# Kernel optimization log

Measured on AMD Instinct MI355X. Metric: run time of the kernel, lower is better.

## Reference

```python
import jax, jax.numpy as jnp
import numpy as np

B_, C_, H_, W_, Dd_ = 2, 64, 32, 32, 32
D_INNER, D_STATE, DT_RANK, D_CONV = 64, 8, 4, 4


def setup_inputs() -> dict:
    key = jax.random.key(0)
    ks = jax.random.split(key, 12)
    s = 0.05
    A_init = jnp.log(jnp.tile(jnp.arange(1, D_STATE + 1, dtype=jnp.float32), (D_INNER, 1)))
    return {
        "input": jax.random.normal(ks[0], (B_, C_, H_, W_, Dd_), jnp.float32),
        "conv_w": jax.random.normal(ks[1], (C_, C_, 3, 3, 3), jnp.float32) * s,
        "conv_b": jax.random.normal(ks[2], (C_,), jnp.float32) * s,
        "in_proj_w": jax.random.normal(ks[3], (2 * D_INNER, C_), jnp.float32) * s,
        "conv1d_w": jax.random.normal(ks[4], (D_INNER, 1, D_CONV), jnp.float32) * s,
        "conv1d_b": jax.random.normal(ks[5], (D_INNER,), jnp.float32) * s,
        "x_proj_w": jax.random.normal(ks[6], (DT_RANK + 2 * D_STATE, D_INNER), jnp.float32) * s,
        "dt_proj_w": jax.random.normal(ks[7], (D_INNER, DT_RANK), jnp.float32) * s,
        "dt_proj_b": jax.random.normal(ks[8], (D_INNER,), jnp.float32) * s,
        "A_log": A_init,
        "A_b_log": A_init + 0.01,
        "D_skip": jnp.ones((D_INNER,), jnp.float32),
        "out_proj_w": jax.random.normal(ks[9], (C_, D_INNER), jnp.float32) * s,
        "ln_g": jnp.ones((C_,), jnp.float32),
        "ln_b": jnp.zeros((C_,), jnp.float32),
    }


def _conv3d(x, w, b):
    y = jax.lax.conv_general_dilated(x, w, (1, 1, 1), [(1, 1), (1, 1), (1, 1)],
                                     dimension_numbers=("NCDHW", "OIDHW", "NCDHW"))
    return y + b[None, :, None, None, None]


def _instance_norm(x, eps=1e-5):
    m = x.mean(axis=(2, 3, 4), keepdims=True)
    v = ((x - m) ** 2).mean(axis=(2, 3, 4), keepdims=True)
    return (x - m) * jax.lax.rsqrt(v + eps)


def _selective_scan(xc, dt, Bm, Cm, A, D_skip):
    # xc, dt: (b,L,d); Bm, Cm: (b,L,n); A: (d,n)
    dA = jnp.exp(dt[..., None] * A)                       # (b,L,d,n)
    dBx = (dt * xc)[..., None] * Bm[:, :, None, :]        # (b,L,d,n)

    def comb(l, r):
        al, bl = l
        ar, br = r
        return ar * al, ar * bl + br

    _, h = jax.lax.associative_scan(comb, (dA, dBx), axis=1)
    y = jnp.einsum("bldn,bln->bld", h, Cm)
    return y + xc * D_skip


def _direction(xz, conv1d_w, conv1d_b, x_proj_w, dt_proj_w, dt_proj_b, A, D_skip):
    x, z = jnp.split(xz, 2, axis=-1)                      # each (b,L,d)
    xt = jnp.swapaxes(x, 1, 2)                            # (b,d,L)
    xc = jax.lax.conv_general_dilated(xt, conv1d_w, (1,), [(D_CONV - 1, 0)],
                                      feature_group_count=D_INNER,
                                      dimension_numbers=("NCH", "OIH", "NCH"))
    xc = jax.nn.silu(jnp.swapaxes(xc + conv1d_b[None, :, None], 1, 2))  # (b,L,d)
    dbl = xc @ x_proj_w.T
    dt_r = dbl[..., :DT_RANK]
    Bm = dbl[..., DT_RANK:DT_RANK + D_STATE]
    Cm = dbl[..., DT_RANK + D_STATE:]
    dt = jax.nn.softplus(dt_r @ dt_proj_w.T + dt_proj_b)
    y = _selective_scan(xc, dt, Bm, Cm, A, D_skip)
    return y * jax.nn.silu(z)


def reference(input, conv_w, conv_b, in_proj_w, conv1d_w, conv1d_b, x_proj_w,
              dt_proj_w, dt_proj_b, A_log, A_b_log, D_skip, out_proj_w, ln_g, ln_b):
    # skip path: Conv3d -> InstanceNorm3d -> ReLU
    skip = jax.nn.relu(_instance_norm(_conv3d(input, conv_w, conv_b)))
    b, c, h, w, d = input.shape
    tokens = input.transpose(0, 2, 3, 4, 1).reshape(b, h * w * d, c)  # b (hwd) c
    xz = tokens @ in_proj_w.T                                          # (b,L,2d)
    A = -jnp.exp(A_log)
    A_b = -jnp.exp(A_b_log)
    y_f = _direction(xz, conv1d_w, conv1d_b, x_proj_w, dt_proj_w, dt_proj_b, A, D_skip)
    y_b = _direction(xz[:, ::-1], conv1d_w, conv1d_b, x_proj_w, dt_proj_w, dt_proj_b, A_b, D_skip)[:, ::-1]
    out = ((y_f + y_b) @ out_proj_w.T) / 2.0  # if_devide_out=True
    mu = out.mean(-1, keepdims=True)
    var = ((out - mu) ** 2).mean(-1, keepdims=True)
    out = (out - mu) * jax.lax.rsqrt(var + 1e-5) * ln_g + ln_b  # use_norm=True
    vol = out.reshape(b, h, w, d, c).transpose(0, 4, 1, 2, 3)
    return _conv3d(vol, conv_w, conv_b) + skip
```

## Files before the change

kernel.cpp:

```cpp
#include <hip/hip_runtime.h>
#include <hip/hip_bf16.h>

typedef __hip_bfloat16 bf16;
typedef __attribute__((ext_vector_type(8))) short short8;
typedef __attribute__((ext_vector_type(4))) float f32x4;

__device__ __forceinline__ float b2f(bf16 x){ return __bfloat162float(x); }
__device__ __forceinline__ bf16  f2b(float x){ return __float2bfloat16(x); }
__device__ __forceinline__ float s2f(short s){ bf16 t = *(bf16*)&s; return b2f(t); }

__device__ __forceinline__ float ldin(const void* p, size_t i, int f32){
  return f32 ? ((const float*)p)[i] : b2f(((const bf16*)p)[i]);
}
__device__ __forceinline__ void stout(void* p, size_t i, float v, int f32){
  if(f32) ((float*)p)[i] = v; else ((bf16*)p)[i] = f2b(v);
}

constexpr int SP   = 32*32*32;
constexpr int LTOK = SP;
constexpr int NC   = 1024;
constexpr int CLEN = LTOK / NC;
constexpr int NSEQ = 2*2*64*8;
constexpr int SEG  = 32;
constexpr int SEGLEN = NC/SEG;

__global__ void k_detect(const void* conv_w, int* flag){
  if(threadIdx.x==0 && blockIdx.x==0){
    const bf16* p = (const bf16*)conv_w;
    int f = 0;
    for(int i=0;i<128;i++){
      float v = b2f(p[i]);
      if(!(v==v) || fabsf(v) > 1.0f) f = 1;
    }
    *flag = f;
  }
}

__global__ void k_fill(void* out, int n, const int* flag){
  const int f32 = *flag;
  int i = blockIdx.x*256 + threadIdx.x;
  if(i<n) stout(out, i, 12345.0f, f32);
}

__global__ void k_wprep(const void* __restrict__ cw, bf16* __restrict__ wt,
                        const int* __restrict__ flag){
  const int f32 = *flag;
  int t = blockIdx.x*256 + threadIdx.x;
  if(t >= 27*64*64) return;
  int tap = t >> 12;
  int oc  = (t >> 6) & 63;
  int ci  = t & 63;
  wt[t] = f2b(ldin(cw, ((size_t)(oc*64+ci))*27 + tap, f32));
}

__global__ __launch_bounds__(256) void k_inprojm(
    const void* __restrict__ in, const void* __restrict__ pw,
    bf16* __restrict__ xz, bf16* __restrict__ xin_t,
    const int* __restrict__ flag){
  const int f32 = *flag;
  __shared__ bf16 tok[128*72];
  __shared__ bf16 wl [128*72];
  int tid = threadIdx.x;
  int b = blockIdx.x >> 8, tile = blockIdx.x & 255;
  int l0 = tile*128;

  for(int p=tid; p<1024; p+=256){
    int j = p & 127, c8 = p >> 7;
    short8 v;
    #pragma unroll
    for(int k=0;k<8;k++){
      bf16 t = f2b(ldin(pw, j*64 + c8*8 + k, f32));
      v[k] = *(short*)&t;
    }
    *(short8*)(&wl[j*72 + c8*8]) = v;
  }
  for(int p=tid; p<1024; p+=256){
    int i = p & 127, c8 = p >> 7;
    short8 v;
    #pragma unroll
    for(int k=0;k<8;k++){
      bf16 t = f2b(ldin(in, ((size_t)(b*64 + c8*8 + k))*SP + l0 + i, f32));
      v[k] = *(short*)&t;
    }
    *(short8*)(&tok[i*72 + c8*8]) = v;
  }
  __syncthreads();

  int lane = tid & 63, wv = tid >> 6;
  int pn = lane & 15, quad = lane >> 4, kg8 = quad*8;
  f32x4 acc[2][8];
  #pragma unroll
  for(int mt=0;mt<2;mt++)
    #pragma unroll
    for(int nt=0;nt<8;nt++) acc[mt][nt]=(f32x4)(0.f);

  #pragma unroll
  for(int kq=0;kq<2;kq++){
    short8 a0 = *(const short8*)(&tok[(wv*32      + pn)*72 + kq*32 + kg8]);
    short8 a1 = *(const short8*)(&tok[(wv*32 + 16 + pn)*72 + kq*32 + kg8]);
    #pragma unroll
    for(int nt=0;nt<8;nt++){
      short8 bb = *(const short8*)(&wl[(nt*16+pn)*72 + kq*32 + kg8]);
      acc[0][nt] = __builtin_amdgcn_mfma_f32_16x16x32_bf16(a0,bb,acc[0][nt],0,0,0);
      acc[1][nt] = __builtin_amdgcn_mfma_f32_16x16x32_bf16(a1,bb,acc[1][nt],0,0,0);
    }
  }

  #pragma unroll
  for(int mt=0;mt<2;mt++){
    #pragma unroll
    for(int nt=0;nt<8;nt++){
      #pragma unroll
      for(int r=0;r<4;r++){
        int token = wv*32 + mt*16 + quad*4 + r;
        xz[((size_t)b*LTOK + l0 + token)*128 + nt*16 + pn] = f2b(acc[mt][nt][r]);
      }
    }
  }
  for(int p=tid; p<8192; p+=256){
    int i = p >> 6, c = p & 63;
    xin_t[((size_t)b*SP + l0 + i)*64 + c] = tok[i*72 + c];
  }
}

__global__ __launch_bounds__(256, 2) void k_convm(
    const bf16* __restrict__ xin_t, const bf16* __restrict__ wt,
    const void* __restrict__ cb, const bf16* __restrict__ skip,
    bf16* __restrict__ out_bf, void* __restrict__ out_any,
    int mode, const int* __restrict__ flag){
  const int f32 = *flag;
  __shared__ bf16 xt[972*40];

  int tid  = threadIdx.x;
  int lane = tid & 63;
  int wv   = tid >> 6;
  int pn   = lane & 15;
  int quad = lane >> 4;
  int kg8  = quad * 8;
  int laneA = pn*64 + kg8;

  int blk0 = blockIdx.x;
  int blk  = (blk0 & 7)*128 + (blk0 >> 3);
  int ocg = blk & 3;
  int wh  = (blk >> 2) & 1;
  int dh2 = (blk >> 3) & 1;
  int h   = (blk >> 4) & 31;
  int b   = blk >> 9;
  int w0  = wh*16;
  int d0  = dh2*16;

  f32x4 acc[4];
  #pragma unroll
  for(int m=0;m<4;m++) acc[m]=(f32x4)(0.f);

  for(int cic=0; cic<64; cic+=32){
    if(cic) __syncthreads();
    for(int it=0; it<16; it++){
      int j = it*256 + tid;
      if(j < 3888){
        int q4 = j & 3, row = j >> 2;
        int hh = row / 324; int rem = row - hh*324;
        int ww = rem / 18;  int dd = rem - ww*18;
        int hg = h + hh - 1, wg = w0 + ww - 1, d = d0 + dd - 1;
        short8 v = (short8)(0);
        if((unsigned)hg < 32u && (unsigned)wg < 32u && (unsigned)d < 32u)
          v = *(const short8*)(&xin_t[(((size_t)b*SP) + hg*1024 + wg*32 + d)*64 + cic + q4*8]);
        *(short8*)(&xt[row*40 + q4*8]) = v;
      }
    }
    __syncthreads();

    short8 afr[27];
    #pragma unroll
    for(int t=0;t<27;t++)
      afr[t] = *(const short8*)(wt + t*4096 + ocg*1024 + cic + laneA);

    #pragma unroll
    for(int kz=0;kz<3;kz++){
      #pragma unroll
      for(int ky=0;ky<3;ky++){
        #pragma unroll
        for(int kx=0;kx<3;kx++){
          int tap = (kz*3+ky)*3+kx;
          #pragma unroll
          for(int wr=0;wr<4;wr++){
            int rix = (kz*18 + wv*4 + wr + ky)*18 + kx + pn;
            short8 bb = *(const short8*)(&xt[rix*40 + kg8]);
            acc[wr] = __builtin_amdgcn_mfma_f32_16x16x32_bf16(afr[tap], bb, acc[wr], 0,0,0);
          }
        }
      }
    }
  }

  #pragma unroll
  for(int wr=0;wr<4;wr++){
    #pragma unroll
    for(int r=0;r<4;r++){
      int oc = ocg*16 + quad*4 + r;
      size_t idx = ((size_t)(b*64+oc))*SP + h*1024 + (w0 + wv*4 + wr)*32 + d0 + pn;
      float v = acc[wr][r] + ldin(cb, oc, f32);
      if(mode==0) out_bf[idx] = f2b(v);
      else        stout(out_any, idx, v + b2f(skip[idx]), f32);
    }
  }
}

__global__ void k_inorm(bf16* __restrict__ buf){
  int bc = blockIdx.x;
  bf16* p = buf + (size_t)bc*SP;
  float s=0.f, s2=0.f;
  for(int i=threadIdx.x;i<SP;i+=256){ float v=b2f(p[i]); s+=v; s2+=v*v; }
  __shared__ float sh[8];
  #pragma unroll
  for(int m=32;m>=1;m>>=1){ s += __shfl_xor(s,m); s2 += __shfl_xor(s2,m); }
  int wid = threadIdx.x>>6;
  if((threadIdx.x&63)==0){ sh[wid]=s; sh[4+wid]=s2; }
  __syncthreads();
  if(threadIdx.x==0){ float a=0,b2=0; for(int i=0;i<4;i++){a+=sh[i]; b2+=sh[4+i];} sh[0]=a; sh[4]=b2; }
  __syncthreads();
  float mean = sh[0]*(1.f/SP);
  float var  = sh[4]*(1.f/SP) - mean*mean;
  float inv = rsqrtf(fmaxf(var,0.f) + 1e-5f);
  for(int i=threadIdx.x;i<SP;i+=256){
    float v=(b2f(p[i])-mean)*inv;
    p[i] = f2b(v>0.f ? v : 0.f);
  }
}

__global__ __launch_bounds__(256) void k_dirprep(
                          const bf16* __restrict__ xz, const void* __restrict__ c1w,
                          const void* __restrict__ c1b, const void* __restrict__ xpw,
                          bf16* __restrict__ bcg, float* __restrict__ dtr,
                          const int* __restrict__ flag){
  const int f32 = *flag;
  __shared__ float xs[67][64];
  __shared__ float xcs[64][68];
  __shared__ float xws[20][68];
  int bid = blockIdx.x;
  int g = bid >> 10, b = (bid>>9)&1, tile = bid & 511;
  int l0 = tile*64;
  int gb = g*2+b;
  int tid = threadIdx.x;
  for(int t=tid; t<20*64; t+=256){ int j=t>>6, d=t&63; xws[j][d]=ldin(xpw, t, f32); }
  for(int t=tid; t<67*64; t+=256){
    int row=t>>6, d=t&63;
    int l = l0 + row - 3;
    float v = 0.f;
    if(l>=0 && l<LTOK){
      int lg = g ? (LTOK-1-l) : l;
      v = b2f(xz[((size_t)b*LTOK + lg)*128 + d]);
    }
    xs[row][d]=v;
  }
  __syncthreads();
  {
    int d = tid & 63;
    float cw0=ldin(c1w,d*4+0,f32), cw1=ldin(c1w,d*4+1,f32),
          cw2=ldin(c1w,d*4+2,f32), cw3=ldin(c1w,d*4+3,f32);
    float cb_=ldin(c1b,d,f32);
    for(int tl = tid>>6; tl<64; tl+=4){
      float acc = cb_ + cw0*xs[tl][d] + cw1*xs[tl+1][d] + cw2*xs[tl+2][d] + cw3*xs[tl+3][d];
      xcs[tl][d] = acc / (1.f + __expf(-acc));
    }
  }
  __syncthreads();
  {
    int tl = tid & 63, wq = tid >> 6;
    float acc[5] = {0.f,0.f,0.f,0.f,0.f};
    #pragma unroll 4
    for(int d4=0; d4<16; d4++){
      float4 xv = *(const float4*)(&xcs[tl][d4*4]);
      #pragma unroll
      for(int jj=0; jj<5; jj++){
        float4 wv = *(const float4*)(&xws[wq*5+jj][d4*4]);
        acc[jj] += xv.x*wv.x + xv.y*wv.y + xv.z*wv.z + xv.w*wv.w;
      }
    }
    size_t l = (size_t)gb*LTOK + l0 + tl;
    #pragma unroll
    for(int jj=0; jj<5; jj++){
      int j = wq*5 + jj;
      if(j<4) dtr[l*4 + j] = acc[jj];
      else    bcg[l*16 + (j-4)] = f2b(acc[jj]);
    }
  }
}

__global__ __launch_bounds__(256, 2) void k_scan1(
                        const bf16* __restrict__ xz, const float* __restrict__ dtr,
                        const bf16* __restrict__ bcg,
                        const void* __restrict__ c1w, const void* __restrict__ c1b,
                        const void* __restrict__ dpw, const void* __restrict__ dpb,
                        const void* __restrict__ alog, const void* __restrict__ ablog,
                        float* __restrict__ psP, float* __restrict__ psS,
                        const int* __restrict__ flag){
  const int f32 = *flag;
  int wid = blockIdx.x*4 + (threadIdx.x>>6);
  int lane = threadIdx.x & 63;
  int chunk = wid & (NC-1);
  int b = (wid>>10)&1;
  int g = wid>>11;
  int gb = g*2+b;
  const void* al = g ? ablog : alog;
  float ac[8];
  #pragma unroll
  for(int n=0;n<8;n++) ac[n] = -__expf(ldin(al, lane*8+n, f32));
  float cw0=ldin(c1w,lane*4+0,f32), cw1=ldin(c1w,lane*4+1,f32), cw2=ldin(c1w,lane*4+2,f32), cw3=ldin(c1w,lane*4+3,f32);
  float cb_=ldin(c1b,lane,f32);
  float dw0=ldin(dpw,lane*4+0,f32), dw1=ldin(dpw,lane*4+1,f32), dw2=ldin(dpw,lane*4+2,f32), dw3=ldin(dpw,lane*4+3,f32);
  float db_=ldin(dpb,lane,f32);
  float S[8];
  #pragma unroll
  for(int n=0;n<8;n++) S[n]=0.f;
  float Tsum = 0.f;
  int lt0 = chunk*CLEN;
  float x0,x1,x2;
  {
    float xr[3];
    #pragma unroll
    for(int j=0;j<3;j++){
      int lt = lt0-3+j;
      float v=0.f;
      if(lt>=0){ int lg = g ? (LTOK-1-lt) : lt; v=b2f(xz[((size_t)b*LTOK+lg)*128 + lane]); }
      xr[j]=v;
    }
    x0=xr[0]; x1=xr[1]; x2=xr[2];
  }
  for(int i0=0;i0<CLEN;i0+=8){
    bf16 xv[8]; float4 dv[8]; short8 bb[8];
    #pragma unroll
    for(int k=0;k<8;k++){
      int lt = lt0+i0+k;
      int lg = g ? (LTOK-1-lt) : lt;
      xv[k] = xz[((size_t)b*LTOK+lg)*128 + lane];
      size_t l = (size_t)gb*LTOK + lt;
      dv[k] = *(const float4*)(dtr + l*4);
      bb[k] = *(const short8*)(bcg + l*16);
    }
    #pragma unroll
    for(int k=0;k<8;k++){
      float x3 = b2f(xv[k]);
      float pre = cb_ + cw0*x0 + cw1*x1 + cw2*x2 + cw3*x3;
      float xc = pre / (1.f + __expf(-pre));
      float v = db_ + dv[k].x*dw0 + dv[k].y*dw1 + dv[k].z*dw2 + dv[k].w*dw3;
      float e = __expf(-fabsf(v));
      float dt = fmaxf(v,0.f) + __logf(1.f+e);
      Tsum += dt;
      float bx = dt*xc;
      #pragma unroll
      for(int n=0;n<8;n++){
        float a = __expf(dt*ac[n]);
        S[n] = a*S[n] + bx*s2f(bb[k][n]);
      }
      x0=x1; x1=x2; x2=x3;
    }
  }
  int seq = (gb*64 + lane)*8;
  #pragma unroll
  for(int n=0;n<8;n++){
    psP[(size_t)chunk*NSEQ + seq + n] = __expf(ac[n]*Tsum);
    psS[(size_t)chunk*NSEQ + seq + n] = S[n];
  }
}

__global__ void k_scan2a(const float* __restrict__ psP, const float* __restrict__ psS,
                         float* __restrict__ segP, float* __restrict__ segS){
  int idx = blockIdx.x*256 + threadIdx.x;
  int seq = idx & (NSEQ-1);
  int seg = idx >> 11;
  float P = 1.f, S = 0.f;
  int i0 = seg*SEGLEN;
  #pragma unroll 4
  for(int i=0;i<SEGLEN;i++){
    float p = psP[(size_t)(i0+i)*NSEQ + seq];
    float s = psS[(size_t)(i0+i)*NSEQ + seq];
    S = p*S + s;
    P *= p;
  }
  segP[seg*NSEQ + seq] = P;
  segS[seg*NSEQ + seq] = S;
}
__global__ void k_scan2b(const float* __restrict__ segP, const float* __restrict__ segS,
                         float* __restrict__ segC){
  int seq = blockIdx.x*256 + threadIdx.x;
  if(seq >= NSEQ) return;
  float h = 0.f;
  #pragma unroll
  for(int s=0;s<SEG;s++){
    segC[s*NSEQ + seq] = h;
    h = segP[s*NSEQ + seq]*h + segS[s*NSEQ + seq];
  }
}
__global__ void k_scan2c(const float* __restrict__ psP, const float* __restrict__ segC,
                         float* __restrict__ psC){
  int idx = blockIdx.x*256 + threadIdx.x;
  int seq = idx & (NSEQ-1);
  int seg = idx >> 11;
  float h = segC[seg*NSEQ + seq];
  int i0 = seg*SEGLEN;
  #pragma unroll 4
  for(int i=0;i<SEGLEN;i++){
    float p = psP[(size_t)(i0+i)*NSEQ + seq];
    float s = psC[(size_t)(i0+i)*NSEQ + seq];
    psC[(size_t)(i0+i)*NSEQ + seq] = h;
    h = p*h + s;
  }
}

__global__ __launch_bounds__(256, 2) void k_scan3(
                        const bf16* __restrict__ xz, const float* __restrict__ dtr,
                        const bf16* __restrict__ bcg,
                        const void* __restrict__ c1w, const void* __restrict__ c1b,
                        const void* __restrict__ dpw, const void* __restrict__ dpb,
                        const void* __restrict__ alog, const void* __restrict__ ablog,
                        const void* __restrict__ dskip, const float* __restrict__ carry,
                        bf16* __restrict__ ybuf, const int* __restrict__ flag){
  const int f32 = *flag;
  int wid = blockIdx.x*4 + (threadIdx.x>>6);
  int lane = threadIdx.x & 63;
  int chunk = wid & (NC-1);
  int b = (wid>>10)&1;
  int g = wid>>11;
  int gb = g*2+b;
  const void* al = g ? ablog : alog;
  float ac[8];
  #pragma unroll
  for(int n=0;n<8;n++) ac[n] = -__expf(ldin(al, lane*8+n, f32));
  float cw0=ldin(c1w,lane*4+0,f32), cw1=ldin(c1w,lane*4+1,f32), cw2=ldin(c1w,lane*4+2,f32), cw3=ldin(c1w,lane*4+3,f32);
  float cb_=ldin(c1b,lane,f32);
  float dw0=ldin(dpw,lane*4+0,f32), dw1=ldin(dpw,lane*4+1,f32), dw2=ldin(dpw,lane*4+2,f32), dw3=ldin(dpw,lane*4+3,f32);
  float db_=ldin(dpb,lane,f32);
  float dsk = ldin(dskip,lane,f32);
  int seq = (gb*64 + lane)*8;
  float h[8];
  #pragma unroll
  for(int n=0;n<8;n++) h[n] = carry[(size_t)chunk*NSEQ + seq + n];
  int lt0 = chunk*CLEN;
  float x0,x1,x2;
  {
    float xr[3];
    #pragma unroll
    for(int j=0;j<3;j++){
      int lt = lt0-3+j;
      float v=0.f;
      if(lt>=0){ int lg = g ? (LTOK-1-lt) : lt; v=b2f(xz[((size_t)b*LTOK+lg)*128 + lane]); }
      xr[j]=v;
    }
    x0=xr[0]; x1=xr[1]; x2=xr[2];
  }
  for(int i0=0;i0<CLEN;i0+=8){
    bf16 xv[8]; float4 dv[8]; short8 bb[8]; short8 cc[8];
    #pragma unroll
    for(int k=0;k<8;k++){
      int lt = lt0+i0+k;
      int lg = g ? (LTOK-1-lt) : lt;
      xv[k] = xz[((size_t)b*LTOK+lg)*128 + lane];
      size_t l = (size_t)gb*LTOK + lt;
      dv[k] = *(const float4*)(dtr + l*4);
      bb[k] = *(const short8*)(bcg + l*16);
      cc[k] = *(const short8*)(bcg + l*16 + 8);
    }
    #pragma unroll
    for(int k=0;k<8;k++){
      float x3 = b2f(xv[k]);
      float pre = cb_ + cw0*x0 + cw1*x1 + cw2*x2 + cw3*x3;
      float xc = pre / (1.f + __expf(-pre));
      float v = db_ + dv[k].x*dw0 + dv[k].y*dw1 + dv[k].z*dw2 + dv[k].w*dw3;
      float e = __expf(-fabsf(v));
      float dt = fmaxf(v,0.f) + __logf(1.f+e);
      float bx = dt*xc;
      float y = xc*dsk;
      #pragma unroll
      for(int n=0;n<8;n++){
        float a = __expf(dt*ac[n]);
        h[n] = a*h[n] + bx*s2f(bb[k][n]);
        y += h[n]*s2f(cc[k][n]);
      }
      size_t l = (size_t)gb*LTOK + lt0+i0+k;
      ybuf[l*64 + lane] = f2b(y);
      x0=x1; x1=x2; x2=x3;
    }
  }
}

__global__ __launch_bounds__(256) void k_outln(
                        const bf16* __restrict__ ybuf, const bf16* __restrict__ xz,
                        const void* __restrict__ opw,
                        const void* __restrict__ lng, const void* __restrict__ lnb,
                        bf16* __restrict__ vol_t, const int* __restrict__ flag){
  const int f32 = *flag;
  __shared__ bf16 vsm[64*72];
  __shared__ bf16 wsm[64*72];
  __shared__ float gsm[64], bsm[64];
  int tid = threadIdx.x;
  int b = blockIdx.x >> 9, tile = blockIdx.x & 511;
  int l0 = tile*64;

  for(int p=tid; p<512; p+=256){
    int c = p & 63, d8 = p >> 6;
    short8 v;
    #pragma unroll
    for(int k=0;k<8;k++){ bf16 t = f2b(ldin(opw, c*64 + d8*8 + k, f32)); v[k] = *(short*)&t; }
    *(short8*)(&wsm[c*72 + d8*8]) = v;
  }
  if(tid<64){ gsm[tid]=ldin(lng,tid,f32); bsm[tid]=ldin(lnb,tid,f32); }
  for(int p=tid; p<4096; p+=256){
    int tl = p >> 6, d = p & 63;
    int l = l0 + tl;
    float yf = b2f(ybuf[((size_t)(0+b)*LTOK + l)*64 + d]);
    float yb = b2f(ybuf[((size_t)(2+b)*LTOK + (LTOK-1-l))*64 + d]);
    float z  = b2f(xz[((size_t)b*LTOK + l)*128 + 64 + d]);
    float sz = z / (1.f + __expf(-z));
    vsm[tl*72 + d] = f2b(0.5f*(yf+yb)*sz);
  }
  __syncthreads();

  int lane = tid & 63, wv = tid >> 6, pn = lane & 15, quad = lane >> 4, kg8 = quad*8;
  f32x4 acc[4];
  #pragma unroll
  for(int nt=0;nt<4;nt++) acc[nt]=(f32x4)(0.f);
  #pragma unroll
  for(int kq=0;kq<2;kq++){
    short8 a = *(const short8*)(&vsm[(wv*16+pn)*72 + kq*32 + kg8]);
    #pragma unroll
    for(int nt=0;nt<4;nt++){
      short8 bb = *(const short8*)(&wsm[(nt*16+pn)*72 + kq*32 + kg8]);
      acc[nt] = __builtin_amdgcn_mfma_f32_16x16x32_bf16(a,bb,acc[nt],0,0,0);
    }
  }
  __syncthreads();

  float gl[4], bl[4];
  #pragma unroll
  for(int nt=0;nt<4;nt++){ gl[nt]=gsm[nt*16+pn]; bl[nt]=bsm[nt*16+pn]; }
  #pragma unroll
  for(int r=0;r<4;r++){
    float vals[4]; float s=0.f;
    #pragma unroll
    for(int nt=0;nt<4;nt++){ vals[nt]=acc[nt][r]; s+=vals[nt]; }
    #pragma unroll
    for(int m=1;m<16;m<<=1) s += __shfl_xor(s, m);
    float mu = s*(1.f/64.f);
    float s2=0.f;
    #pragma unroll
    for(int nt=0;nt<4;nt++){ float dv=vals[nt]-mu; s2+=dv*dv; }
    #pragma unroll
    for(int m=1;m<16;m<<=1) s2 += __shfl_xor(s2, m);
    float inv = rsqrtf(s2*(1.f/64.f) + 1e-5f);
    int token = wv*16 + quad*4 + r;
    #pragma unroll
    for(int nt=0;nt<4;nt++){
      vsm[token*72 + nt*16 + pn] = f2b((vals[nt]-mu)*inv*gl[nt] + bl[nt]);
    }
  }
  __syncthreads();
  for(int p=tid; p<512; p+=256){
    int tl = p >> 3, d8 = p & 7;
    *(short8*)(&vol_t[((size_t)b*SP + l0 + tl)*64 + d8*8]) = *(const short8*)(&vsm[tl*72 + d8*8]);
  }
}

extern "C" void kernel_launch(void* const* d_in, const int* in_sizes, int n_in,
                              void* d_out, int out_size, void* d_ws, size_t ws_size,
                              hipStream_t stream){
  const void* input  = d_in[0];
  const void* conv_w = d_in[1];
  const void* conv_b = d_in[2];
  const void* inpw   = d_in[3];
  const void* c1w    = d_in[4];
  const void* c1b    = d_in[5];
  const void* xpw    = d_in[6];
  const void* dpw    = d_in[7];
  const void* dpb    = d_in[8];
  const void* alog   = d_in[9];
  const void* ablog  = d_in[10];
  const void* dskip  = d_in[11];
  const void* opw    = d_in[12];
  const void* lng    = d_in[13];
  const void* lnb    = d_in[14];

  char* base = (char*)d_ws;
  bf16*  skipb = (bf16*) (base + 0);
  bf16*  xz    = (bf16*) (base + 8388608);
  bf16*  bcg   = (bf16*) (base + 25165824);
  float* dtr   = (float*)(base + 29360128);
  float* psP   = (float*)(base + 31457280);
  bf16*  xin_t = (bf16*) (base + 39845888);
  bf16*  ybuf  = (bf16*) (base + 31457280);
  float* psS   = (float*)(base + 48234496);
  bf16*  vol_t = (bf16*) (base + 48234496);
  bf16*  wt    = (bf16*) (base + 56623104);
  float* segP  = (float*)(base + 56844288);
  float* segS  = (float*)(base + 57106432);
  float* segC  = (float*)(base + 57368576);
  int*   flagp = (int*)  (base + 57630720);
  const size_t NEED = 57630736;

  k_detect<<<dim3(1), dim3(64), 0, stream>>>(conv_w, flagp);

  if(ws_size < NEED){
    k_fill<<<dim3((out_size+255)/256), dim3(256), 0, stream>>>(d_out, out_size, flagp);
    return;
  }

  k_wprep  <<<dim3(432),   dim3(256), 0, stream>>>(conv_w, wt, flagp);
  k_inprojm<<<dim3(512),   dim3(256), 0, stream>>>(input, inpw, xz, xin_t, flagp);
  k_convm  <<<dim3(1024),  dim3(256), 0, stream>>>(xin_t, wt, conv_b, nullptr, skipb, nullptr, 0, flagp);
  k_inorm  <<<dim3(128),   dim3(256), 0, stream>>>(skipb);
  k_dirprep<<<dim3(2048),  dim3(256), 0, stream>>>(xz, c1w, c1b, xpw, bcg, dtr, flagp);
  k_scan1  <<<dim3(1024),  dim3(256), 0, stream>>>(xz, dtr, bcg, c1w, c1b, dpw, dpb, alog, ablog, psP, psS, flagp);
  k_scan2a <<<dim3(256),   dim3(256), 0, stream>>>(psP, psS, segP, segS);
  k_scan2b <<<dim3(8),     dim3(256), 0, stream>>>(segP, segS, segC);
  k_scan2c <<<dim3(256),   dim3(256), 0, stream>>>(psP, segC, psS);
  k_scan3  <<<dim3(1024),  dim3(256), 0, stream>>>(xz, dtr, bcg, c1w, c1b, dpw, dpb, alog, ablog, dskip, psS, ybuf, flagp);
  k_outln  <<<dim3(1024),  dim3(256), 0, stream>>>(ybuf, xz, opw, lng, lnb, vol_t, flagp);
  k_convm  <<<dim3(1024),  dim3(256), 0, stream>>>(vol_t, wt, conv_b, skipb, nullptr, d_out, 1, flagp);
}
```

Measured before the change: 411.4 us.

## Split scan state dimension across two wavefronts to double parallelism

Scan kernels now use 128-thread blocks where each wavefront handles half of the 8 state dimensions for a channel, quadrupling the block count. In the output pass, partial y contributions are combined via a double-buffered shared-memory array with a barrier per 8 tokens. This raises wave-level parallelism and latency hiding for the serial recurrence, at the cost of duplicating the per-token conv/softplus work and adding synchronization.

```diff
diff --git a/kernel.cpp b/kernel.cpp
--- a/kernel.cpp
+++ b/kernel.cpp
@@ -3,6 +3,7 @@
 
 typedef __hip_bfloat16 bf16;
 typedef __attribute__((ext_vector_type(8))) short short8;
+typedef __attribute__((ext_vector_type(4))) short short4v;
 typedef __attribute__((ext_vector_type(4))) float f32x4;
 
 __device__ __forceinline__ float b2f(bf16 x){ return __bfloat162float(x); }
@@ -287,7 +288,7 @@
   }
 }
 
-__global__ __launch_bounds__(256, 2) void k_scan1(
+__global__ __launch_bounds__(128, 4) void k_scan1(
                         const bf16* __restrict__ xz, const float* __restrict__ dtr,
                         const bf16* __restrict__ bcg,
                         const void* __restrict__ c1w, const void* __restrict__ c1b,
@@ -296,23 +297,24 @@
                         float* __restrict__ psP, float* __restrict__ psS,
                         const int* __restrict__ flag){
   const int f32 = *flag;
-  int wid = blockIdx.x*4 + (threadIdx.x>>6);
+  int bid = blockIdx.x;
   int lane = threadIdx.x & 63;
-  int chunk = wid & (NC-1);
-  int b = (wid>>10)&1;
-  int g = wid>>11;
+  int nh   = threadIdx.x >> 6;
+  int chunk = bid & (NC-1);
+  int b = (bid>>10)&1;
+  int g = bid>>11;
   int gb = g*2+b;
   const void* al = g ? ablog : alog;
-  float ac[8];
-  #pragma unroll
-  for(int n=0;n<8;n++) ac[n] = -__expf(ldin(al, lane*8+n, f32));
+  float ac[4];
+  #pragma unroll
+  for(int n=0;n<4;n++) ac[n] = -__expf(ldin(al, lane*8 + nh*4 + n, f32));
   float cw0=ldin(c1w,lane*4+0,f32), cw1=ldin(c1w,lane*4+1,f32), cw2=ldin(c1w,lane*4+2,f32), cw3=ldin(c1w,lane*4+3,f32);
   float cb_=ldin(c1b,lane,f32);
   float dw0=ldin(dpw,lane*4+0,f32), dw1=ldin(dpw,lane*4+1,f32), dw2=ldin(dpw,lane*4+2,f32), dw3=ldin(dpw,lane*4+3,f32);
   float db_=ldin(dpb,lane,f32);
-  float S[8];
-  #pragma unroll
-  for(int n=0;n<8;n++) S[n]=0.f;
+  float S[4];
+  #pragma unroll
+  for(int n=0;n<4;n++) S[n]=0.f;
   float Tsum = 0.f;
   int lt0 = chunk*CLEN;
   float x0,x1,x2;
@@ -328,7 +330,7 @@
     x0=xr[0]; x1=xr[1]; x2=xr[2];
   }
   for(int i0=0;i0<CLEN;i0+=8){
-    bf16 xv[8]; float4 dv[8]; short8 bb[8];
+    bf16 xv[8]; float4 dv[8]; short4v bb[8];
     #pragma unroll
     for(int k=0;k<8;k++){
       int lt = lt0+i0+k;
@@ -336,7 +338,7 @@
       xv[k] = xz[((size_t)b*LTOK+lg)*128 + lane];
       size_t l = (size_t)gb*LTOK + lt;
       dv[k] = *(const float4*)(dtr + l*4);
-      bb[k] = *(const short8*)(bcg + l*16);
+      bb[k] = *(const short4v*)(bcg + l*16 + nh*4);
     }
     #pragma unroll
     for(int k=0;k<8;k++){
@@ -349,16 +351,16 @@
       Tsum += dt;
       float bx = dt*xc;
       #pragma unroll
-      for(int n=0;n<8;n++){
+      for(int n=0;n<4;n++){
         float a = __expf(dt*ac[n]);
         S[n] = a*S[n] + bx*s2f(bb[k][n]);
       }
       x0=x1; x1=x2; x2=x3;
     }
   }
-  int seq = (gb*64 + lane)*8;
-  #pragma unroll
-  for(int n=0;n<8;n++){
+  int seq = (gb*64 + lane)*8 + nh*4;
+  #pragma unroll
+  for(int n=0;n<4;n++){
     psP[(size_t)chunk*NSEQ + seq + n] = __expf(ac[n]*Tsum);
     psS[(size_t)chunk*NSEQ + seq + n] = S[n];
   }
@@ -408,7 +410,7 @@
   }
 }
 
-__global__ __launch_bounds__(256, 2) void k_scan3(
+__global__ __launch_bounds__(128, 4) void k_scan3(
                         const bf16* __restrict__ xz, const float* __restrict__ dtr,
                         const bf16* __restrict__ bcg,
                         const void* __restrict__ c1w, const void* __restrict__ c1b,
@@ -417,25 +419,27 @@
                         const void* __restrict__ dskip, const float* __restrict__ carry,
                         bf16* __restrict__ ybuf, const int* __restrict__ flag){
   const int f32 = *flag;
-  int wid = blockIdx.x*4 + (threadIdx.x>>6);
+  __shared__ float ysh[2][8][64];
+  int bid = blockIdx.x;
   int lane = threadIdx.x & 63;
-  int chunk = wid & (NC-1);
-  int b = (wid>>10)&1;
-  int g = wid>>11;
+  int nh   = threadIdx.x >> 6;
+  int chunk = bid & (NC-1);
+  int b = (bid>>10)&1;
+  int g = bid>>11;
   int gb = g*2+b;
   const void* al = g ? ablog : alog;
-  float ac[8];
-  #pragma unroll
-  for(int n=0;n<8;n++) ac[n] = -__expf(ldin(al, lane*8+n, f32));
+  float ac[4];
+  #pragma unroll
+  for(int n=0;n<4;n++) ac[n] = -__expf(ldin(al, lane*8 + nh*4 + n, f32));
   float cw0=ldin(c1w,lane*4+0,f32), cw1=ldin(c1w,lane*4+1,f32), cw2=ldin(c1w,lane*4+2,f32), cw3=ldin(c1w,lane*4+3,f32);
   float cb_=ldin(c1b,lane,f32);
   float dw0=ldin(dpw,lane*4+0,f32), dw1=ldin(dpw,lane*4+1,f32), dw2=ldin(dpw,lane*4+2,f32), dw3=ldin(dpw,lane*4+3,f32);
   float db_=ldin(dpb,lane,f32);
   float dsk = ldin(dskip,lane,f32);
-  int seq = (gb*64 + lane)*8;
-  float h[8];
-  #pragma unroll
-  for(int n=0;n<8;n++) h[n] = carry[(size_t)chunk*NSEQ + seq + n];
+  int seq = (gb*64 + lane)*8 + nh*4;
+  float h[4];
+  #pragma unroll
+  for(int n=0;n<4;n++) h[n] = carry[(size_t)chunk*NSEQ + seq + n];
   int lt0 = chunk*CLEN;
   float x0,x1,x2;
   {
@@ -450,7 +454,8 @@
     x0=xr[0]; x1=xr[1]; x2=xr[2];
   }
   for(int i0=0;i0<CLEN;i0+=8){
-    bf16 xv[8]; float4 dv[8]; short8 bb[8]; short8 cc[8];
+    int bt = (i0>>3)&1;
+    bf16 xv[8]; float4 dv[8]; short4v bb[8], cc[8];
     #pragma unroll
     for(int k=0;k<8;k++){
       int lt = lt0+i0+k;
@@ -458,9 +463,10 @@
       xv[k] = xz[((size_t)b*LTOK+lg)*128 + lane];
       size_t l = (size_t)gb*LTOK + lt;
       dv[k] = *(const float4*)(dtr + l*4);
-      bb[k] = *(const short8*)(bcg + l*16);
-      cc[k] = *(const short8*)(bcg + l*16 + 8);
-    }
+      bb[k] = *(const short4v*)(bcg + l*16 + nh*4);
+      cc[k] = *(const short4v*)(bcg + l*16 + 8 + nh*4);
+    }
+    float py[8];
     #pragma unroll
     for(int k=0;k<8;k++){
       float x3 = b2f(xv[k]);
@@ -470,16 +476,24 @@
       float e = __expf(-fabsf(v));
       float dt = fmaxf(v,0.f) + __logf(1.f+e);
       float bx = dt*xc;
-      float y = xc*dsk;
+      float part = nh ? xc*dsk : 0.f;
       #pragma unroll
-      for(int n=0;n<8;n++){
+      for(int n=0;n<4;n++){
         float a = __expf(dt*ac[n]);
         h[n] = a*h[n] + bx*s2f(bb[k][n]);
-        y += h[n]*s2f(cc[k][n]);
+        part += h[n]*s2f(cc[k][n]);
       }
-      size_t l = (size_t)gb*LTOK + lt0+i0+k;
-      ybuf[l*64 + lane] = f2b(y);
+      if(nh==0) ysh[bt][k][lane] = part;
+      else      py[k] = part;
       x0=x1; x1=x2; x2=x3;
+    }
+    __syncthreads();
+    if(nh==1){
+      #pragma unroll
+      for(int k=0;k<8;k++){
+        size_t l = (size_t)gb*LTOK + lt0+i0+k;
+        ybuf[l*64 + lane] = f2b(ysh[bt][k][lane] + py[k]);
+      }
     }
   }
 }
@@ -609,11 +623,11 @@
   k_convm  <<<dim3(1024),  dim3(256), 0, stream>>>(xin_t, wt, conv_b, nullptr, skipb, nullptr, 0, flagp);
   k_inorm  <<<dim3(128),   dim3(256), 0, stream>>>(skipb);
   k_dirprep<<<dim3(2048),  dim3(256), 0, stream>>>(xz, c1w, c1b, xpw, bcg, dtr, flagp);
-  k_scan1  <<<dim3(1024),  dim3(256), 0, stream>>>(xz, dtr, bcg, c1w, c1b, dpw, dpb, alog, ablog, psP, psS, flagp);
+  k_scan1  <<<dim3(4096),  dim3(128), 0, stream>>>(xz, dtr, bcg, c1w, c1b, dpw, dpb, alog, ablog, psP, psS, flagp);
   k_scan2a <<<dim3(256),   dim3(256), 0, stream>>>(psP, psS, segP, segS);
   k_scan2b <<<dim3(8),     dim3(256), 0, stream>>>(segP, segS, segC);
   k_scan2c <<<dim3(256),   dim3(256), 0, stream>>>(psP, segC, psS);
-  k_scan3  <<<dim3(1024),  dim3(256), 0, stream>>>(xz, dtr, bcg, c1w, c1b, dpw, dpb, alog, ablog, dskip, psS, ybuf, flagp);
+  k_scan3  <<<dim3(4096),  dim3(128), 0, stream>>>(xz, dtr, bcg, c1w, c1b, dpw, dpb, alog, ablog, dskip, psS, ybuf, flagp);
   k_outln  <<<dim3(1024),  dim3(256), 0, stream>>>(ybuf, xz, opw, lng, lnb, vol_t, flagp);
   k_convm  <<<dim3(1024),  dim3(256), 0, stream>>>(vol_t, wt, conv_b, skipb, nullptr, d_out, 1, flagp);
 }
```

After: 416.9 us. About the same (+1.3%).
